# Kernel tuning notes

Hardware: AMD Instinct MI355X
Metric: run time of the kernel (lower is better)

The kernel has to match this reference:

```python
import jax, jax.numpy as jnp
import numpy as np

B, T, E = 2, 4096, 1024
N_HEAD, DIM_HEAD = 16, 64
BUCKET_SIZE, N_HASHES = 64, 4
N_LOCAL = 4
DIM_FF = 4096
TOKEN_SELF_VAL = -5e4
LN_EPS = 1e-5


def _mask_val(dtype):
    return -jnp.finfo(dtype).max


def layer_norm(x, g, b):
    mu = x.mean(-1, keepdims=True)
    var = ((x - mu) ** 2).mean(-1, keepdims=True)
    return (x - mu) / jnp.sqrt(var + LN_EPS) * g + b


def lsh_attend(qk, v, rotations):
    # qk, v: (bh, t, d). Faithful port of reformer_pytorch LSHAttention
    # (causal, attend_across_buckets=True, allow_duplicate_attention=True).
    bh, t, d = qk.shape
    nb = t // BUCKET_SIZE  # n_buckets
    # --- hash vectors ---
    rotated = jnp.einsum('btf,fhi->bhti', qk, rotations)  # (bh,H,t,nb//2)
    rotated = jnp.concatenate([rotated, -rotated], axis=-1)
    buckets = jnp.argmax(rotated, axis=-1)  # (bh,H,t)
    offsets = (jnp.arange(N_HASHES) * nb).reshape(1, -1, 1)
    buckets = (buckets + offsets).reshape(bh, -1)  # (bh, H*t)
    # --- sort by (bucket, time) ---
    ticker = jnp.arange(N_HASHES * t)
    buckets_and_t = t * buckets + (ticker[None, :] % t)
    sticker = jnp.argsort(buckets_and_t, axis=-1)  # (bh, H*t)
    undo = jnp.argsort(sticker, axis=-1)
    st = sticker % t
    sqk = jnp.take_along_axis(qk, st[:, :, None], axis=1)
    sv = jnp.take_along_axis(v, st[:, :, None], axis=1)
    chunks = N_HASHES * nb
    bq_t = st.reshape(bh, chunks, BUCKET_SIZE)
    bqk = sqk.reshape(bh, chunks, BUCKET_SIZE, d)
    bv = sv.reshape(bh, chunks, BUCKET_SIZE, d)
    bq = bqk
    bk = bqk / jnp.linalg.norm(bqk, axis=-1, keepdims=True)  # normalize keys

    def look_one_back(x):
        extra = jnp.concatenate([x[:, -1:], x[:, :-1]], axis=1)
        return jnp.concatenate([x, extra], axis=2)

    bk = look_one_back(bk)
    bv = look_one_back(bv)
    bkv_t = look_one_back(bq_t)
    dots = jnp.einsum('bcie,bcje->bcij', bq, bk) * (d ** -0.5)
    mval = _mask_val(dots.dtype)
    dots = jnp.where(bq_t[:, :, :, None] < bkv_t[:, :, None, :], mval, dots)  # causal
    dots = jnp.where(bq_t[:, :, :, None] == bkv_t[:, :, None, :], TOKEN_SELF_VAL, dots)
    lse = jax.scipy.special.logsumexp(dots, axis=-1, keepdims=True)
    p = jnp.exp(dots - lse)
    bo = jnp.einsum('bcij,bcje->bcie', p, bv)
    so = bo.reshape(bh, -1, d)
    slog = lse.reshape(bh, -1)
    o = jnp.take_along_axis(so, undo[:, :, None], axis=1)
    logits = jnp.take_along_axis(slog, undo, axis=1)
    o = o.reshape(bh, N_HASHES, t, d)
    logits = logits.reshape(bh, N_HASHES, t, 1)
    probs = jnp.exp(logits - jax.scipy.special.logsumexp(logits, axis=1, keepdims=True))
    return jnp.sum(o * probs, axis=1)  # (bh, t, d)


def local_attend(q, k, v):
    # local-attention with shared_qk=True, causal, window=2*bucket_size,
    # look_backward=1, look_forward=0.
    b, t, e = q.shape
    w = 2 * BUCKET_SIZE
    nw = t // w
    k = k / jnp.linalg.norm(k, axis=-1, keepdims=True)
    b_t = jnp.arange(t).reshape(1, nw, w)
    bq = q.reshape(b, nw, w, e)
    bk = k.reshape(b, nw, w, e)
    bv = v.reshape(b, nw, w, e)

    def look_around(x, pad_value):
        pads = [(0, 0), (1, 0)] + [(0, 0)] * (x.ndim - 2)
        padded = jnp.pad(x, pads, constant_values=pad_value)
        return jnp.concatenate([padded[:, :-1], padded[:, 1:]], axis=2)  # [prev, cur]

    bk = look_around(bk, 0.0)
    bv = look_around(bv, 0.0)
    bq_k = look_around(b_t, -1)
    dots = jnp.einsum('bwie,bwje->bwij', bq, bk) * (e ** -0.5)
    mval = _mask_val(dots.dtype)
    dots = jnp.where(b_t[:, :, :, None] == bq_k[:, :, None, :], TOKEN_SELF_VAL, dots)
    dots = jnp.where(b_t[:, :, :, None] < bq_k[:, :, None, :], mval, dots)
    dots = jnp.where((bq_k == -1)[:, :, None, :], mval, dots)
    attn = jax.nn.softmax(dots, axis=-1)
    out = jnp.einsum('bwij,bwje->bwie', attn, bv)
    return out.reshape(b, t, e)


def _block(x, w_qk, w_v, w_out, b_out, w_ff1, b_ff1, w_ff2, b_ff2,
           ln1_g, ln1_b, ln2_g, ln2_b, rotations):
    b, t, e = x.shape
    qk = x @ w_qk.T
    v = x @ w_v.T
    # split heads: (b,t,e) -> (b,h,t,dh)
    qk = qk.reshape(b, t, N_HEAD, DIM_HEAD).transpose(0, 2, 1, 3)
    v = v.reshape(b, t, N_HEAD, DIM_HEAD).transpose(0, 2, 1, 3)
    lsh_h = N_HEAD - N_LOCAL
    lqk = qk[:, :N_LOCAL].reshape(b * N_LOCAL, t, DIM_HEAD)
    lv = v[:, :N_LOCAL].reshape(b * N_LOCAL, t, DIM_HEAD)
    qk_l = qk[:, N_LOCAL:].reshape(b * lsh_h, t, DIM_HEAD)
    v_l = v[:, N_LOCAL:].reshape(b * lsh_h, t, DIM_HEAD)
    out_lsh = lsh_attend(qk_l, v_l, rotations).reshape(b, lsh_h, t, DIM_HEAD)
    out_loc = local_attend(lqk, lqk, lv).reshape(b, N_LOCAL, t, DIM_HEAD)
    out = jnp.concatenate([out_loc, out_lsh], axis=1)  # local heads first
    out = out.transpose(0, 2, 1, 3).reshape(b, t, e)
    sa = out @ w_out.T + b_out
    x = layer_norm(x + sa, ln1_g, ln1_b)
    h = jax.nn.gelu(x @ w_ff1.T + b_ff1, approximate=False)
    ff = h @ w_ff2.T + b_ff2
    return layer_norm(x + ff, ln2_g, ln2_b)


def setup_inputs() -> dict:
    key = jax.random.key(0)
    ks = jax.random.split(key, 8)
    s = 0.02
    return {
        'x': jax.random.normal(ks[0], (B, T, E), jnp.float32),
        'w_qk': s * jax.random.normal(ks[1], (E, E), jnp.float32),
        'w_v': s * jax.random.normal(ks[2], (E, E), jnp.float32),
        'w_out': s * jax.random.normal(ks[3], (E, E), jnp.float32),
        'b_out': jnp.zeros((E,), jnp.float32),
        'w_ff1': s * jax.random.normal(ks[4], (DIM_FF, E), jnp.float32),
        'b_ff1': jnp.zeros((DIM_FF,), jnp.float32),
        'w_ff2': s * jax.random.normal(ks[5], (E, DIM_FF), jnp.float32),
        'b_ff2': jnp.zeros((E,), jnp.float32),
        'ln1_g': jnp.ones((E,), jnp.float32),
        'ln1_b': jnp.zeros((E,), jnp.float32),
        'ln2_g': jnp.ones((E,), jnp.float32),
        'ln2_b': jnp.zeros((E,), jnp.float32),
        'rotations': jax.random.normal(ks[6], (DIM_HEAD, N_HASHES, (T // BUCKET_SIZE) // 2), jnp.float32),
    }


def reference(x, w_qk, w_v, w_out, b_out, w_ff1, b_ff1, w_ff2, b_ff2,
              ln1_g, ln1_b, ln2_g, ln2_b, rotations):
    return _block(x, w_qk, w_v, w_out, b_out, w_ff1, b_ff1, w_ff2, b_ff2,
                  ln1_g, ln1_b, ln2_g, ln2_b, rotations)
```

## Files before the change

kernel.cpp:

```cpp
#include <hip/hip_runtime.h>
#include <math.h>


#define TSEQ 4096
#define EMB  1024
#define HT   16384
#define GAP_EPS 1.2e-5f

__device__ __forceinline__ ushort f2bf_rne(float f) {
  unsigned int u = __float_as_uint(f);
  u += 0x7fffu + ((u >> 16) & 1u);
  return (ushort)(u >> 16);
}
__device__ __forceinline__ float bf2f(ushort h) {
  return __uint_as_float(((unsigned int)h) << 16);
}

typedef __attribute__((ext_vector_type(8))) short bfrag8;
typedef __attribute__((ext_vector_type(4))) float accf4;

__device__ __forceinline__ void glds16(const ushort* g, ushort* l) {
  __builtin_amdgcn_global_load_lds(
      (const __attribute__((address_space(1))) unsigned int*)g,
      (__attribute__((address_space(3))) unsigned int*)l, 16, 0, 0);
}

__global__ __launch_bounds__(256) void split2_kernel(
    const float4* __restrict__ s, ushort4* __restrict__ h,
    ushort4* __restrict__ l, int n4) {
  int i = blockIdx.x * 256 + threadIdx.x;
  int st = gridDim.x * 256;
  for (; i < n4; i += st) {
    float4 v = s[i];
    ushort4 hh, ll;
    hh.x = f2bf_rne(v.x); ll.x = f2bf_rne(v.x - bf2f(hh.x));
    hh.y = f2bf_rne(v.y); ll.y = f2bf_rne(v.y - bf2f(hh.y));
    hh.z = f2bf_rne(v.z); ll.z = f2bf_rne(v.z - bf2f(hh.z));
    hh.w = f2bf_rne(v.w); ll.w = f2bf_rne(v.w - bf2f(hh.w));
    h[i] = hh; l[i] = ll;
  }
}

__global__ __launch_bounds__(256) void split3_kernel(
    const float4* __restrict__ s, ushort4* __restrict__ h,
    ushort4* __restrict__ m, ushort4* __restrict__ l, int n4) {
  int i = blockIdx.x * 256 + threadIdx.x;
  int st = gridDim.x * 256;
  for (; i < n4; i += st) {
    float4 v = s[i];
    ushort4 hh, mm, ll;
    {
      ushort a = f2bf_rne(v.x); float r = v.x - bf2f(a);
      ushort b = f2bf_rne(r);   float r2 = r - bf2f(b);
      hh.x = a; mm.x = b; ll.x = f2bf_rne(r2);
    }
    {
      ushort a = f2bf_rne(v.y); float r = v.y - bf2f(a);
      ushort b = f2bf_rne(r);   float r2 = r - bf2f(b);
      hh.y = a; mm.y = b; ll.y = f2bf_rne(r2);
    }
    {
      ushort a = f2bf_rne(v.z); float r = v.z - bf2f(a);
      ushort b = f2bf_rne(r);   float r2 = r - bf2f(b);
      hh.z = a; mm.z = b; ll.z = f2bf_rne(r2);
    }
    {
      ushort a = f2bf_rne(v.w); float r = v.w - bf2f(a);
      ushort b = f2bf_rne(r);   float r2 = r - bf2f(b);
      hh.w = a; mm.w = b; ll.w = f2bf_rne(r2);
    }
    h[i] = hh; m[i] = mm; l[i] = ll;
  }
}

#define SSTR 136

template<int AT, int BT, int MS, bool BIAS, bool GELU_ACT, bool F32OUT, bool BF16OUT>
__global__ __launch_bounds__(256) void gemm_mfma_bt(
    const ushort* __restrict__ A0, const ushort* __restrict__ A1,
    const ushort* __restrict__ A2,
    const ushort* __restrict__ B0, const ushort* __restrict__ B1,
    const ushort* __restrict__ B2,
    const float* __restrict__ bias, float* __restrict__ C,
    ushort* __restrict__ Cbf,
    int M, int N, int K) {
  constexpr int NMAT = AT + BT;
  constexpr int LDSU0 = NMAT * 4096;
  constexpr int LDSU = (BF16OUT && LDSU0 < 128 * SSTR) ? 128 * SSTR : LDSU0;
  __shared__ ushort smu[LDSU];

  const ushort* As[3] = {A0, A1, A2};
  const ushort* Bs[3] = {B0, B1, B2};

  int tid = threadIdx.x;
  int lane = tid & 63, wave = tid >> 6;

  int bx, by;
  {
    int gx = gridDim.x, gy = gridDim.y;
    int nwg = gx * gy;
    int flat = blockIdx.y * gx + blockIdx.x;
    if ((nwg & 7) == 0 && (gx & 3) == 0 && (gy & 3) == 0) {
      int cpx = nwg >> 3;
      int id = (flat & 7) * cpx + (flat >> 3);
      int sid = id >> 4, within = id & 15;
      int scols = gx >> 2;
      int srow = sid / scols, scol = sid - srow * scols;
      by = srow * 4 + (within >> 2);
      bx = scol * 4 + (within & 3);
    } else {
      bx = blockIdx.x; by = blockIdx.y;
    }
  }
  int m0 = by * 128, n0 = bx * 128;
  int wr = wave >> 1, wc = wave & 1;

  accf4 acc[4][4];
#pragma unroll
  for (int i = 0; i < 4; ++i)
#pragma unroll
    for (int j = 0; j < 4; ++j)
      acc[i][j] = (accf4){0.f, 0.f, 0.f, 0.f};

  int lr = lane & 15, kb = lane >> 4;
  int arow = wr * 64 + lr;
  int brow = wc * 64 + lr;

  int srowL = lane >> 2;
  int scolL = (lane & 3) * 8;

  constexpr int CH = NMAT * 8;
  int nk = K / 32;
  for (int kt = 0; kt < nk; ++kt) {
    int koff = kt * 32;
#pragma unroll
    for (int c = wave; c < CH; c += 4) {
      int mat = c >> 3, sub = c & 7;
      const ushort* src;
      if (mat < AT)
        src = As[mat] + (size_t)(m0 + sub * 16 + srowL) * K + koff + scolL;
      else
        src = Bs[mat - AT] + (size_t)(n0 + sub * 16 + srowL) * K + koff + scolL;
      glds16(src, smu + c * 512);
    }
    __syncthreads();

    bfrag8 af[AT][4], bf[BT][4];
#pragma unroll
    for (int t = 0; t < AT; ++t)
#pragma unroll
      for (int i = 0; i < 4; ++i)
        af[t][i] = *(const bfrag8*)&smu[t * 4096 + (arow + i * 16) * 32 + kb * 8];
#pragma unroll
    for (int t = 0; t < BT; ++t)
#pragma unroll
      for (int i = 0; i < 4; ++i)
        bf[t][i] = *(const bfrag8*)&smu[(AT + t) * 4096 + (brow + i * 16) * 32 + kb * 8];
#pragma unroll
    for (int p = 0; p < AT; ++p)
#pragma unroll
      for (int q = 0; q < BT; ++q) {
        if (p + q <= MS) {
#pragma unroll
          for (int i = 0; i < 4; ++i)
#pragma unroll
            for (int j = 0; j < 4; ++j)
              acc[i][j] = __builtin_amdgcn_mfma_f32_16x16x32_bf16(
                  af[p][i], bf[q][j], acc[i][j], 0, 0, 0);
        }
      }
    __syncthreads();
  }

  int crow = (lane >> 4) * 4;
  int ccol = lane & 15;
  if (!BF16OUT) {
#pragma unroll
    for (int i = 0; i < 4; ++i) {
#pragma unroll
      for (int j = 0; j < 4; ++j) {
#pragma unroll
        for (int r = 0; r < 4; ++r) {
          int m = m0 + wr * 64 + i * 16 + crow + r;
          int n = n0 + wc * 64 + j * 16 + ccol;
          float val = acc[i][j][r];
          if (BIAS) val += bias[n];
          if (GELU_ACT) val = 0.5f * val * (1.f + erff(val * 0.70710678118654752f));
          if (F32OUT) C[(size_t)m * N + n] = val;
        }
      }
    }
  } else {
    ushort* stg = smu;
#pragma unroll
    for (int i = 0; i < 4; ++i) {
#pragma unroll
      for (int j = 0; j < 4; ++j) {
#pragma unroll
        for (int r = 0; r < 4; ++r) {
          int ml = wr * 64 + i * 16 + crow + r;
          int nl = wc * 64 + j * 16 + ccol;
          float val = acc[i][j][r];
          if (BIAS) val += bias[n0 + nl];
          if (GELU_ACT) val = 0.5f * val * (1.f + erff(val * 0.70710678118654752f));
          stg[ml * SSTR + nl] = f2bf_rne(val);
        }
      }
    }
    __syncthreads();
    int rowl = tid >> 1, half = tid & 1;
    const uint4* src = (const uint4*)(stg + rowl * SSTR + half * 64);
    uint4* dst = (uint4*)(Cbf + (size_t)(m0 + rowl) * N + n0 + half * 64);
#pragma unroll
    for (int u = 0; u < 8; ++u) dst[u] = src[u];
  }
}

__global__ __launch_bounds__(256) void hash_kernel(
    const float* __restrict__ qk, const float* __restrict__ rot,
    int* __restrict__ buckets, int* __restrict__ altb,
    float* __restrict__ gapf) {
  int idx = blockIdx.x * 256 + threadIdx.x;
  int t = idx & 4095;
  int bh_h = idx >> 12;
  int h = bh_h & 3;
  int bh = bh_h >> 2;
  int b = bh / 12, hh = bh % 12;
  const float* qrow = qk + ((size_t)(b * TSEQ + t) * EMB + (4 + hh) * 64);
  double q[64]; double qn2 = 0.0;
#pragma unroll
  for (int f = 0; f < 64; ++f) { q[f] = (double)qrow[f]; qn2 += q[f] * q[f]; }
  double r[32];
  for (int i = 0; i < 32; ++i) {
    double acc = 0.0;
#pragma unroll
    for (int f = 0; f < 64; ++f)
      acc = fma(q[f], (double)rot[f * 128 + h * 32 + i], acc);
    r[i] = acc;
  }
  double best1 = -1e300, best2 = -1e300; int j1 = 0, j2 = 0;
  for (int j = 0; j < 64; ++j) {
    double val = (j < 32) ? r[j] : -r[j - 32];
    if (val > best1) { best2 = best1; j2 = j1; best1 = val; j1 = j; }
    else if (val > best2) { best2 = val; j2 = j; }
  }
  buckets[idx] = j1 + h * 64;
  altb[idx]    = j2 + h * 64;
  gapf[idx] = (float)((best1 - best2) / sqrt(qn2 + 1e-300));
}

__global__ __launch_bounds__(256) void mkalt_kernel(
    const int* __restrict__ buckets, const int* __restrict__ altb,
    const float* __restrict__ gapf, int* __restrict__ buckets1) {
  int idx = blockIdx.x * 256 + threadIdx.x;
  buckets1[idx] = (gapf[idx] < GAP_EPS) ? altb[idx] : buckets[idx];
}

__global__ __launch_bounds__(64) void sort_kernel(
    const int* __restrict__ buckets, int* __restrict__ stime,
    int* __restrict__ undo) {
  int bh = blockIdx.x >> 8;
  int bucket = blockIdx.x & 255;
  int h = bucket >> 6;
  int lane = threadIdx.x;
  const int* row = buckets + (size_t)bh * HT;
  int cnt = 0;
  for (int base = 0; base < HT; base += 64)
    cnt += (row[base + lane] < bucket) ? 1 : 0;
#pragma unroll
  for (int off = 1; off < 64; off <<= 1) cnt += __shfl_xor(cnt, off);
  int offset = cnt;
  const int* hrow = row + h * 4096;
  for (int t0 = 0; t0 < 4096; t0 += 64) {
    bool match = (hrow[t0 + lane] == bucket);
    unsigned long long m = __ballot(match);
    int pre = __popcll(m & ((1ull << lane) - 1ull));
    if (match) {
      int pos = offset + pre;
      int time = t0 + lane;
      stime[(size_t)bh * HT + pos] = time;
      undo[(size_t)bh * HT + h * 4096 + time] = pos;
    }
    offset += __popcll(m);
  }
}

#define KSTR  88
#define VSTR 152

__global__ __launch_bounds__(256) void lsh_attend_mfma_kernel(
    const float* __restrict__ qk, const float* __restrict__ v,
    const int* __restrict__ stime, float* __restrict__ so,
    float* __restrict__ slog) {
  __shared__ ushort KS[128 * KSTR];
  __shared__ ushort VT[64 * VSTR];
  __shared__ int tks[128];
  __shared__ float qn[64];
  ushort* PS = KS;

  int bh = blockIdx.x >> 8;
  int c = blockIdx.x & 255;
  int prev = (c + 255) & 255;
  int b = bh / 12, hh = bh % 12;
  int col0 = (4 + hh) * 64;
  int tid = threadIdx.x;
  int lane = tid & 63;
  int wave = tid >> 6;

  if (tid < 128) {
    int src = (tid < 64) ? c : prev;
    tks[tid] = stime[(size_t)bh * HT + src * 64 + (tid & 63)];
  }
  __syncthreads();

  if (tid < 128) {
    int r = tid;
    const float* kr = qk + (size_t)(b * TSEQ + tks[r]) * EMB + col0;
    float row[64]; float ss = 0.f;
#pragma unroll
    for (int f = 0; f < 64; f += 4) {
      float4 t4 = *(const float4*)(kr + f);
      row[f] = t4.x; row[f + 1] = t4.y; row[f + 2] = t4.z; row[f + 3] = t4.w;
      ss += t4.x * t4.x + t4.y * t4.y + t4.z * t4.z + t4.w * t4.w;
    }
    float rn = (ss > 0.f) ? rsqrtf(ss) : 0.f;
    if (r < 64) qn[r] = sqrtf(ss);
#pragma unroll
    for (int f = 0; f < 64; f += 4) {
      ushort4 u;
      u.x = f2bf_rne(row[f] * rn);
      u.y = f2bf_rne(row[f + 1] * rn);
      u.z = f2bf_rne(row[f + 2] * rn);
      u.w = f2bf_rne(row[f + 3] * rn);
      *(ushort4*)&KS[r * KSTR + f] = u;
    }
  } else {
    int kk = tid - 128;
    const float* vr = v + (size_t)(b * TSEQ + tks[kk]) * EMB + col0;
#pragma unroll
    for (int f = 0; f < 64; f += 4) {
      float4 t4 = *(const float4*)(vr + f);
      VT[(f + 0) * VSTR + kk] = f2bf_rne(t4.x);
      VT[(f + 1) * VSTR + kk] = f2bf_rne(t4.y);
      VT[(f + 2) * VSTR + kk] = f2bf_rne(t4.z);
      VT[(f + 3) * VSTR + kk] = f2bf_rne(t4.w);
    }
  }
  __syncthreads();

  int lr = lane & 15, kb = lane >> 4;
  int qrow0 = wave * 16;
  bfrag8 af0 = *(const bfrag8*)&KS[(qrow0 + lr) * KSTR + kb * 8];
  bfrag8 af1 = *(const bfrag8*)&KS[(qrow0 + lr) * KSTR + 32 + kb * 8];
  float d[8][4];
#pragma unroll
  for (int nt = 0; nt < 8; ++nt) {
    bfrag8 b0 = *(const bfrag8*)&KS[(nt * 16 + lr) * KSTR + kb * 8];
    bfrag8 b1 = *(const bfrag8*)&KS[(nt * 16 + lr) * KSTR + 32 + kb * 8];
    accf4 acc = (accf4){0.f, 0.f, 0.f, 0.f};
    acc = __builtin_amdgcn_mfma_f32_16x16x32_bf16(af0, b0, acc, 0, 0, 0);
    acc = __builtin_amdgcn_mfma_f32_16x16x32_bf16(af1, b1, acc, 0, 0, 0);
#pragma unroll
    for (int r = 0; r < 4; ++r) d[nt][r] = acc[r];
  }

  const float mvalf = -3.402823466e38f;
  int crow = kb * 4;
  int tq[4]; float qs[4];
#pragma unroll
  for (int r = 0; r < 4; ++r) {
    tq[r] = tks[qrow0 + crow + r];
    qs[r] = qn[qrow0 + crow + r] * 0.125f;
  }
  float mrow[4] = {mvalf, mvalf, mvalf, mvalf};
#pragma unroll
  for (int nt = 0; nt < 8; ++nt) {
    int tk = tks[nt * 16 + lr];
#pragma unroll
    for (int r = 0; r < 4; ++r) {
      float dv = d[nt][r] * qs[r];
      if (tq[r] < tk) dv = mvalf;
      else if (tq[r] == tk) dv = -5e4f;
      d[nt][r] = dv;
      mrow[r] = fmaxf(mrow[r], dv);
    }
  }
#pragma unroll
  for (int off = 1; off < 16; off <<= 1)
#pragma unroll
    for (int r = 0; r < 4; ++r)
      mrow[r] = fmaxf(mrow[r], __shfl_xor(mrow[r], off));
  float srow[4] = {0.f, 0.f, 0.f, 0.f};
#pragma unroll
  for (int nt = 0; nt < 8; ++nt)
#pragma unroll
    for (int r = 0; r < 4; ++r) {
      float e = expf(d[nt][r] - mrow[r]);
      d[nt][r] = e;
      srow[r] += e;
    }
#pragma unroll
  for (int off = 1; off < 16; off <<= 1)
#pragma unroll
    for (int r = 0; r < 4; ++r)
      srow[r] += __shfl_xor(srow[r], off);
  if (lr == 0) {
#pragma unroll
    for (int r = 0; r < 4; ++r) {
      size_t orow = (size_t)bh * HT + c * 64 + qrow0 + crow + r;
      slog[orow] = mrow[r] + logf(srow[r]);
    }
  }
  float inv[4];
#pragma unroll
  for (int r = 0; r < 4; ++r) inv[r] = 1.f / srow[r];

  __syncthreads();
#pragma unroll
  for (int nt = 0; nt < 8; ++nt)
#pragma unroll
    for (int r = 0; r < 4; ++r)
      PS[(qrow0 + crow + r) * VSTR + nt * 16 + lr] = f2bf_rne(d[nt][r] * inv[r]);
  __syncthreads();

  bfrag8 ap[4];
#pragma unroll
  for (int ks = 0; ks < 4; ++ks)
    ap[ks] = *(const bfrag8*)&PS[(qrow0 + lr) * VSTR + ks * 32 + kb * 8];
#pragma unroll
  for (int nt = 0; nt < 4; ++nt) {
    accf4 acc = (accf4){0.f, 0.f, 0.f, 0.f};
#pragma unroll
    for (int ks = 0; ks < 4; ++ks) {
      bfrag8 bv = *(const bfrag8*)&VT[(nt * 16 + lr) * VSTR + ks * 32 + kb * 8];
      acc = __builtin_amdgcn_mfma_f32_16x16x32_bf16(ap[ks], bv, acc, 0, 0, 0);
    }
#pragma unroll
    for (int r = 0; r < 4; ++r) {
      size_t orow = (size_t)bh * HT + c * 64 + qrow0 + crow + r;
      so[orow * 64 + nt * 16 + lr] = acc[r];
    }
  }
}

__global__ __launch_bounds__(256) void lsh_combine_kernel(
    const float* __restrict__ so, const float* __restrict__ slog,
    const int* __restrict__ undo, float* __restrict__ attn,
    float wnew, float wold) {
  int idx = blockIdx.x * 4 + (threadIdx.x >> 6);
  int lane = threadIdx.x & 63;
  int bh = idx >> 12;
  int t = idx & 4095;
  int b = bh / 12, hh = bh % 12;
  float l[4]; int pos[4];
#pragma unroll
  for (int h = 0; h < 4; ++h) {
    pos[h] = undo[(size_t)bh * HT + h * 4096 + t];
    l[h] = slog[(size_t)bh * HT + pos[h]];
  }
  float m = fmaxf(fmaxf(l[0], l[1]), fmaxf(l[2], l[3]));
  float w[4], s = 0.f;
#pragma unroll
  for (int h = 0; h < 4; ++h) { w[h] = expf(l[h] - m); s += w[h]; }
  float inv = 1.f / s;
  float o = 0.f;
#pragma unroll
  for (int h = 0; h < 4; ++h)
    o += w[h] * inv * so[((size_t)bh * HT + pos[h]) * 64 + lane];
  size_t oi = (size_t)(b * TSEQ + t) * EMB + (4 + hh) * 64 + lane;
  attn[oi] = wold * attn[oi] + wnew * o;
}

#define LKSTR  72
#define LVSTR 264
#define LPSTR 264

__global__ __launch_bounds__(512) void local_attend_mfma_kernel(
    const float* __restrict__ qk, const float* __restrict__ v,
    float* __restrict__ attn) {
  __shared__ ushort KS[256 * LKSTR];
  __shared__ ushort VT[64 * LVSTR];
  __shared__ ushort PS[128 * LPSTR];
  __shared__ float qn[128];
  int row = blockIdx.x >> 5;
  int win = blockIdx.x & 31;
  int b = row >> 2, hl = row & 3;
  int col0 = hl * 64;
  int tid = threadIdx.x;
  int lane = tid & 63, wave = tid >> 6;

  if (tid < 256) {
    int r = tid;
    int t = (r < 128) ? ((win > 0) ? (win - 1) * 128 + r : -1)
                      : (win * 128 + (r - 128));
    if (t >= 0) {
      const float* kr = qk + (size_t)(b * TSEQ + t) * EMB + col0;
      float rowv[64]; float ss = 0.f;
#pragma unroll
      for (int f = 0; f < 64; f += 4) {
        float4 t4 = *(const float4*)(kr + f);
        rowv[f] = t4.x; rowv[f + 1] = t4.y; rowv[f + 2] = t4.z; rowv[f + 3] = t4.w;
        ss += t4.x * t4.x + t4.y * t4.y + t4.z * t4.z + t4.w * t4.w;
      }
      float rn = (ss > 0.f) ? rsqrtf(ss) : 0.f;
      if (r >= 128) qn[r - 128] = sqrtf(ss);
#pragma unroll
      for (int f = 0; f < 64; f += 4) {
        ushort4 u;
        u.x = f2bf_rne(rowv[f] * rn);
        u.y = f2bf_rne(rowv[f + 1] * rn);
        u.z = f2bf_rne(rowv[f + 2] * rn);
        u.w = f2bf_rne(rowv[f + 3] * rn);
        *(ushort4*)&KS[r * LKSTR + f] = u;
      }
    } else {
      ushort4 z = {0, 0, 0, 0};
#pragma unroll
      for (int f = 0; f < 64; f += 4)
        *(ushort4*)&KS[r * LKSTR + f] = z;
    }
  } else {
    int kk = tid - 256;
    int t = (kk < 128) ? ((win > 0) ? (win - 1) * 128 + kk : -1)
                       : (win * 128 + (kk - 128));
    if (t >= 0) {
      const float* vr = v + (size_t)(b * TSEQ + t) * EMB + col0;
#pragma unroll
      for (int f = 0; f < 64; f += 4) {
        float4 t4 = *(const float4*)(vr + f);
        VT[(f + 0) * LVSTR + kk] = f2bf_rne(t4.x);
        VT[(f + 1) * LVSTR + kk] = f2bf_rne(t4.y);
        VT[(f + 2) * LVSTR + kk] = f2bf_rne(t4.z);
        VT[(f + 3) * LVSTR + kk] = f2bf_rne(t4.w);
      }
    } else {
#pragma unroll
      for (int f = 0; f < 64; ++f) VT[f * LVSTR + kk] = 0;
    }
  }
  __syncthreads();

  int lr = lane & 15, kb = lane >> 4;
  int q0 = wave * 16;
  bfrag8 af0 = *(const bfrag8*)&KS[(128 + q0 + lr) * LKSTR + kb * 8];
  bfrag8 af1 = *(const bfrag8*)&KS[(128 + q0 + lr) * LKSTR + 32 + kb * 8];
  float d[16][4];
#pragma unroll
  for (int nt = 0; nt < 16; ++nt) {
    bfrag8 b0 = *(const bfrag8*)&KS[(nt * 16 + lr) * LKSTR + kb * 8];
    bfrag8 b1 = *(const bfrag8*)&KS[(nt * 16 + lr) * LKSTR + 32 + kb * 8];
    accf4 acc = (accf4){0.f, 0.f, 0.f, 0.f};
    acc = __builtin_amdgcn_mfma_f32_16x16x32_bf16(af0, b0, acc, 0, 0, 0);
    acc = __builtin_amdgcn_mfma_f32_16x16x32_bf16(af1, b1, acc, 0, 0, 0);
#pragma unroll
    for (int r = 0; r < 4; ++r) d[nt][r] = acc[r];
  }

  const float mvalf = -3.402823466e38f;
  int crow = kb * 4;
  int tq[4]; float qs[4];
#pragma unroll
  for (int r = 0; r < 4; ++r) {
    int qi = q0 + crow + r;
    tq[r] = win * 128 + qi;
    qs[r] = qn[qi] * 0.125f;
  }
  float mrow[4] = {mvalf, mvalf, mvalf, mvalf};
#pragma unroll
  for (int nt = 0; nt < 16; ++nt) {
    int slot = nt * 16 + lr;
    int tk = (slot < 128) ? ((win > 0) ? (win - 1) * 128 + slot : -1)
                          : (win * 128 + (slot - 128));
#pragma unroll
    for (int r = 0; r < 4; ++r) {
      float dv = d[nt][r] * qs[r];
      if (tk < 0) dv = mvalf;
      else if (tq[r] == tk) dv = -5e4f;
      else if (tq[r] < tk) dv = mvalf;
      d[nt][r] = dv;
      mrow[r] = fmaxf(mrow[r], dv);
    }
  }
#pragma unroll
  for (int off = 1; off < 16; off <<= 1)
#pragma unroll
    for (int r = 0; r < 4; ++r)
      mrow[r] = fmaxf(mrow[r], __shfl_xor(mrow[r], off));
  float srow[4] = {0.f, 0.f, 0.f, 0.f};
#pragma unroll
  for (int nt = 0; nt < 16; ++nt)
#pragma unroll
    for (int r = 0; r < 4; ++r) {
      float e = expf(d[nt][r] - mrow[r]);
      d[nt][r] = e;
      srow[r] += e;
    }
#pragma unroll
  for (int off = 1; off < 16; off <<= 1)
#pragma unroll
    for (int r = 0; r < 4; ++r)
      srow[r] += __shfl_xor(srow[r], off);
  float inv[4];
#pragma unroll
  for (int r = 0; r < 4; ++r) inv[r] = 1.f / srow[r];

#pragma unroll
  for (int nt = 0; nt < 16; ++nt)
#pragma unroll
    for (int r = 0; r < 4; ++r)
      PS[(q0 + crow + r) * LPSTR + nt * 16 + lr] = f2bf_rne(d[nt][r] * inv[r]);
  __syncthreads();

  bfrag8 ap[8];
#pragma unroll
  for (int ks = 0; ks < 8; ++ks)
    ap[ks] = *(const bfrag8*)&PS[(q0 + lr) * LPSTR + ks * 32 + kb * 8];
#pragma unroll
  for (int nt = 0; nt < 4; ++nt) {
    accf4 acc = (accf4){0.f, 0.f, 0.f, 0.f};
#pragma unroll
    for (int ks = 0; ks < 8; ++ks) {
      bfrag8 bv = *(const bfrag8*)&VT[(nt * 16 + lr) * LVSTR + ks * 32 + kb * 8];
      acc = __builtin_amdgcn_mfma_f32_16x16x32_bf16(ap[ks], bv, acc, 0, 0, 0);
    }
#pragma unroll
    for (int r = 0; r < 4; ++r) {
      int tqw = win * 128 + q0 + crow + r;
      attn[(size_t)(b * TSEQ + tqw) * EMB + col0 + nt * 16 + lr] = acc[r];
    }
  }
}

template<bool SPLIT>
__global__ __launch_bounds__(256) void add_ln_kernel(
    const float* __restrict__ a, const float* __restrict__ bsrc,
    const float* __restrict__ g, const float* __restrict__ beta,
    float* __restrict__ out, ushort* __restrict__ ohi,
    ushort* __restrict__ olo) {
  int row = blockIdx.x;
  int tid = threadIdx.x, lane = tid & 63, wave = tid >> 6;
  const float* pa = a + (size_t)row * EMB;
  const float* pb = bsrc + (size_t)row * EMB;
  float xv[4]; float s = 0.f;
#pragma unroll
  for (int u = 0; u < 4; ++u) { int c = tid + u * 256; xv[u] = pa[c] + pb[c]; s += xv[u]; }
#pragma unroll
  for (int off = 1; off < 64; off <<= 1) s += __shfl_xor(s, off);
  __shared__ float red[4];
  __shared__ float red2[4];
  if (lane == 0) red[wave] = s;
  __syncthreads();
  float mu = (red[0] + red[1] + red[2] + red[3]) * (1.f / 1024.f);
  float vs = 0.f;
#pragma unroll
  for (int u = 0; u < 4; ++u) { float dd = xv[u] - mu; vs += dd * dd; }
#pragma unroll
  for (int off = 1; off < 64; off <<= 1) vs += __shfl_xor(vs, off);
  if (lane == 0) red2[wave] = vs;
  __syncthreads();
  float var = (red2[0] + red2[1] + red2[2] + red2[3]) * (1.f / 1024.f);
  float rstd = rsqrtf(var + 1e-5f);
#pragma unroll
  for (int u = 0; u < 4; ++u) {
    int c = tid + u * 256;
    float val = (xv[u] - mu) * rstd * g[c] + beta[c];
    size_t off = (size_t)row * EMB + c;
    out[off] = val;
    if (SPLIT) {
      ushort hh = f2bf_rne(val);
      ohi[off] = hh;
      olo[off] = f2bf_rne(val - bf2f(hh));
    }
  }
}

extern "C" void kernel_launch(void* const* d_in, const int* in_sizes, int n_in,
                              void* d_out, int out_size, void* d_ws, size_t ws_size,
                              hipStream_t stream) {
  (void)in_sizes; (void)n_in; (void)out_size; (void)ws_size;
  const float* x     = (const float*)d_in[0];
  const float* w_qk  = (const float*)d_in[1];
  const float* w_v   = (const float*)d_in[2];
  const float* w_out = (const float*)d_in[3];
  const float* b_out = (const float*)d_in[4];
  const float* w_ff1 = (const float*)d_in[5];
  const float* b_ff1 = (const float*)d_in[6];
  const float* w_ff2 = (const float*)d_in[7];
  const float* b_ff2 = (const float*)d_in[8];
  const float* ln1_g = (const float*)d_in[9];
  const float* ln1_b = (const float*)d_in[10];
  const float* ln2_g = (const float*)d_in[11];
  const float* ln2_b = (const float*)d_in[12];
  const float* rot   = (const float*)d_in[13];
  float* out = (float*)d_out;

  float* ws = (float*)d_ws;
  const size_t SZ = (size_t)8192 * 1024;
  float* qk   = ws;
  float* v    = ws + SZ;
  float* attn = ws + 2 * SZ;
  float* big  = ws + 3 * SZ;
  float* so   = big;
  float* slog = big + (size_t)24 * HT * 64;
  int*   buckets  = (int*)(slog + (size_t)24 * HT);
  int*   stimep   = buckets + (size_t)24 * HT;
  int*   undop    = stimep + (size_t)24 * HT;
  int*   altb     = undop + (size_t)24 * HT;
  float* gapf     = (float*)(altb + (size_t)24 * HT);
  int*   buckets1 = (int*)(gapf + (size_t)24 * HT);
  float* sa  = qk;
  float* x1  = v;
  float* ffo = attn;

  const size_t M4 = 4194304;
  ushort* xs_h  = (ushort*)big;
  ushort* xs_m  = (ushort*)(big + M4);
  ushort* xs_l  = (ushort*)(big + 2 * M4);
  ushort* wqk_h = (ushort*)(big + 3 * M4);
  ushort* wqk_m = (ushort*)(big + 3 * M4 + 524288);
  ushort* wqk_l = (ushort*)(big + 3 * M4 + 2 * 524288);
  ushort* wv_h  = (ushort*)(big + 3 * M4 + 3 * 524288);
  ushort* wv_l  = (ushort*)(big + 3 * M4 + 4 * 524288);
  ushort* attn_h = (ushort*)big;
  ushort* attn_l = (ushort*)(big + M4);
  ushort* wout_h = (ushort*)v;
  ushort* wout_l = (ushort*)(v + 524288);
  ushort* x1_h  = (ushort*)attn;
  ushort* x1_l  = (ushort*)(attn + M4);
  ushort* wff1_h = (ushort*)qk;
  ushort* wff1_l = (ushort*)(qk + 2097152);
  ushort* wff2_h = (ushort*)(qk + 2 * 2097152);
  ushort* wff2_l = (ushort*)(qk + 3 * 2097152);
  ushort* ffh_h = (ushort*)big;

  dim3 blk256(256), blk64(64), blk512(512);
  dim3 g1024(8, 64), g4096(32, 64);

  split3_kernel<<<2048, blk256, 0, stream>>>((const float4*)x, (ushort4*)xs_h,
      (ushort4*)xs_m, (ushort4*)xs_l, 2097152);
  split3_kernel<<<1024, blk256, 0, stream>>>((const float4*)w_qk, (ushort4*)wqk_h,
      (ushort4*)wqk_m, (ushort4*)wqk_l, 262144);
  split2_kernel<<<1024, blk256, 0, stream>>>((const float4*)w_v, (ushort4*)wv_h,
      (ushort4*)wv_l, 262144);
  gemm_mfma_bt<3, 3, 2, false, false, true, false><<<g1024, blk256, 0, stream>>>(
      xs_h, xs_m, xs_l, wqk_h, wqk_m, wqk_l, nullptr, qk, nullptr,
      8192, 1024, 1024);
  gemm_mfma_bt<2, 2, 1, false, false, true, false><<<g1024, blk256, 0, stream>>>(
      xs_h, xs_m, nullptr, wv_h, wv_l, nullptr, nullptr, v, nullptr,
      8192, 1024, 1024);
  hash_kernel<<<1536, blk256, 0, stream>>>(qk, rot, buckets, altb, gapf);
  mkalt_kernel<<<1536, blk256, 0, stream>>>(buckets, altb, gapf, buckets1);

  sort_kernel<<<6144, blk64, 0, stream>>>(buckets, stimep, undop);
  lsh_attend_mfma_kernel<<<6144, blk256, 0, stream>>>(qk, v, stimep, so, slog);
  lsh_combine_kernel<<<24576, blk256, 0, stream>>>(so, slog, undop, attn, 1.0f, 0.0f);
  sort_kernel<<<6144, blk64, 0, stream>>>(buckets1, stimep, undop);
  lsh_attend_mfma_kernel<<<6144, blk256, 0, stream>>>(qk, v, stimep, so, slog);
  lsh_combine_kernel<<<24576, blk256, 0, stream>>>(so, slog, undop, attn, 0.5f, 0.5f);

  local_attend_mfma_kernel<<<256, blk512, 0, stream>>>(qk, v, attn);

  split2_kernel<<<2048, blk256, 0, stream>>>((const float4*)attn, (ushort4*)attn_h,
      (ushort4*)attn_l, 2097152);
  split2_kernel<<<1024, blk256, 0, stream>>>((const float4*)w_out, (ushort4*)wout_h,
      (ushort4*)wout_l, 262144);
  gemm_mfma_bt<2, 2, 1, true, false, true, false><<<g1024, blk256, 0, stream>>>(
      attn_h, attn_l, nullptr, wout_h, wout_l, nullptr, b_out, sa, nullptr,
      8192, 1024, 1024);
  add_ln_kernel<true><<<8192, blk256, 0, stream>>>(x, sa, ln1_g, ln1_b, x1, x1_h, x1_l);
  split2_kernel<<<2048, blk256, 0, stream>>>((const float4*)w_ff1, (ushort4*)wff1_h,
      (ushort4*)wff1_l, 1048576);
  split2_kernel<<<2048, blk256, 0, stream>>>((const float4*)w_ff2, (ushort4*)wff2_h,
      (ushort4*)wff2_l, 1048576);
  gemm_mfma_bt<2, 2, 1, true, true, false, true><<<g4096, blk256, 0, stream>>>(
      x1_h, x1_l, nullptr, wff1_h, wff1_l, nullptr, b_ff1, nullptr, ffh_h,
      8192, 4096, 1024);
  gemm_mfma_bt<1, 2, 1, true, false, true, false><<<g1024, blk256, 0, stream>>>(
      ffh_h, nullptr, nullptr, wff2_h, wff2_l, nullptr, b_ff2, ffo, nullptr,
      8192, 1024, 4096);
  add_ln_kernel<false><<<8192, blk256, 0, stream>>>(x1, ffo, ln2_g, ln2_b, out,
      nullptr, nullptr);
}
```

Measured before the change: 1.176 ms.

## Emit bf16 qk/v from projections and cut split-precision terms in GEMMs

The QK projection now writes both fp32 and a bf16 copy, and the V projection writes only bf16 with fewer split terms. The LSH and local attention kernels read these bf16 operands directly instead of fp32, which halves their gather traffic and drops the per-element conversions. The output projection and FF1 GEMMs lose one split-precision term (the low part of W_out and of x1), and add_ln no longer writes the low bf16 half. The LSH attention grid is also swizzled so that consecutive blocks spread across heads. The cost is lower precision in several places, which risks failing the accuracy tolerance.

```diff
diff --git a/kernel.cpp b/kernel.cpp
--- a/kernel.cpp
+++ b/kernel.cpp
@@ -203,6 +203,7 @@
           float val = acc[i][j][r];
           if (BIAS) val += bias[n0 + nl];
           if (GELU_ACT) val = 0.5f * val * (1.f + erff(val * 0.70710678118654752f));
+          if (F32OUT) C[(size_t)(m0 + ml) * N + n0 + nl] = val;
           stg[ml * SSTR + nl] = f2bf_rne(val);
         }
       }
@@ -289,7 +290,7 @@
 #define VSTR 152
 
 __global__ __launch_bounds__(256) void lsh_attend_mfma_kernel(
-    const float* __restrict__ qk, const float* __restrict__ v,
+    const ushort* __restrict__ qkb, const ushort* __restrict__ vb,
     const int* __restrict__ stime, float* __restrict__ so,
     float* __restrict__ slog) {
   __shared__ ushort KS[128 * KSTR];
@@ -298,8 +299,9 @@
   __shared__ float qn[64];
   ushort* PS = KS;
 
-  int bh = blockIdx.x >> 8;
-  int c = blockIdx.x & 255;
+  int sw = (blockIdx.x & 7) * 768 + (blockIdx.x >> 3);
+  int bh = sw >> 8;
+  int c = sw & 255;
   int prev = (c + 255) & 255;
   int b = bh / 12, hh = bh % 12;
   int col0 = (4 + hh) * 64;
@@ -315,13 +317,16 @@
 
   if (tid < 128) {
     int r = tid;
-    const float* kr = qk + (size_t)(b * TSEQ + tks[r]) * EMB + col0;
+    const ushort* kr = qkb + (size_t)(b * TSEQ + tks[r]) * EMB + col0;
     float row[64]; float ss = 0.f;
 #pragma unroll
-    for (int f = 0; f < 64; f += 4) {
-      float4 t4 = *(const float4*)(kr + f);
-      row[f] = t4.x; row[f + 1] = t4.y; row[f + 2] = t4.z; row[f + 3] = t4.w;
-      ss += t4.x * t4.x + t4.y * t4.y + t4.z * t4.z + t4.w * t4.w;
+    for (int f = 0; f < 64; f += 8) {
+      uint4 u4 = *(const uint4*)(kr + f);
+      const ushort* us = (const ushort*)&u4;
+#pragma unroll
+      for (int q = 0; q < 8; ++q) {
+        float x = bf2f(us[q]); row[f + q] = x; ss += x * x;
+      }
     }
     float rn = (ss > 0.f) ? rsqrtf(ss) : 0.f;
     if (r < 64) qn[r] = sqrtf(ss);
@@ -336,14 +341,14 @@
     }
   } else {
     int kk = tid - 128;
-    const float* vr = v + (size_t)(b * TSEQ + tks[kk]) * EMB + col0;
-#pragma unroll
-    for (int f = 0; f < 64; f += 4) {
-      float4 t4 = *(const float4*)(vr + f);
-      VT[(f + 0) * VSTR + kk] = f2bf_rne(t4.x);
-      VT[(f + 1) * VSTR + kk] = f2bf_rne(t4.y);
-      VT[(f + 2) * VSTR + kk] = f2bf_rne(t4.z);
-      VT[(f + 3) * VSTR + kk] = f2bf_rne(t4.w);
+    const ushort* vr = vb + (size_t)(b * TSEQ + tks[kk]) * EMB + col0;
+#pragma unroll
+    for (int f = 0; f < 64; f += 8) {
+      uint4 u4 = *(const uint4*)(vr + f);
+      const ushort* us = (const ushort*)&u4;
+#pragma unroll
+      for (int q = 0; q < 8; ++q)
+        VT[(f + q) * VSTR + kk] = us[q];
     }
   }
   __syncthreads();
@@ -476,7 +481,7 @@
 #define LPSTR 264
 
 __global__ __launch_bounds__(512) void local_attend_mfma_kernel(
-    const float* __restrict__ qk, const float* __restrict__ v,
+    const ushort* __restrict__ qkb, const ushort* __restrict__ vb,
     float* __restrict__ attn) {
   __shared__ ushort KS[256 * LKSTR];
   __shared__ ushort VT[64 * LVSTR];
@@ -494,13 +499,16 @@
     int t = (r < 128) ? ((win > 0) ? (win - 1) * 128 + r : -1)
                       : (win * 128 + (r - 128));
     if (t >= 0) {
-      const float* kr = qk + (size_t)(b * TSEQ + t) * EMB + col0;
+      const ushort* kr = qkb + (size_t)(b * TSEQ + t) * EMB + col0;
       float rowv[64]; float ss = 0.f;
 #pragma unroll
-      for (int f = 0; f < 64; f += 4) {
-        float4 t4 = *(const float4*)(kr + f);
-        rowv[f] = t4.x; rowv[f + 1] = t4.y; rowv[f + 2] = t4.z; rowv[f + 3] = t4.w;
-        ss += t4.x * t4.x + t4.y * t4.y + t4.z * t4.z + t4.w * t4.w;
+      for (int f = 0; f < 64; f += 8) {
+        uint4 u4 = *(const uint4*)(kr + f);
+        const ushort* us = (const ushort*)&u4;
+#pragma unroll
+        for (int q = 0; q < 8; ++q) {
+          float x = bf2f(us[q]); rowv[f + q] = x; ss += x * x;
+        }
       }
       float rn = (ss > 0.f) ? rsqrtf(ss) : 0.f;
       if (r >= 128) qn[r - 128] = sqrtf(ss);
@@ -524,14 +532,14 @@
     int t = (kk < 128) ? ((win > 0) ? (win - 1) * 128 + kk : -1)
                        : (win * 128 + (kk - 128));
     if (t >= 0) {
-      const float* vr = v + (size_t)(b * TSEQ + t) * EMB + col0;
-#pragma unroll
-      for (int f = 0; f < 64; f += 4) {
-        float4 t4 = *(const float4*)(vr + f);
-        VT[(f + 0) * LVSTR + kk] = f2bf_rne(t4.x);
-        VT[(f + 1) * LVSTR + kk] = f2bf_rne(t4.y);
-        VT[(f + 2) * LVSTR + kk] = f2bf_rne(t4.z);
-        VT[(f + 3) * LVSTR + kk] = f2bf_rne(t4.w);
+      const ushort* vr = vb + (size_t)(b * TSEQ + t) * EMB + col0;
+#pragma unroll
+      for (int f = 0; f < 64; f += 8) {
+        uint4 u4 = *(const uint4*)(vr + f);
+        const ushort* us = (const ushort*)&u4;
+#pragma unroll
+        for (int q = 0; q < 8; ++q)
+          VT[(f + q) * LVSTR + kk] = us[q];
       }
     } else {
 #pragma unroll
@@ -635,8 +643,7 @@
 __global__ __launch_bounds__(256) void add_ln_kernel(
     const float* __restrict__ a, const float* __restrict__ bsrc,
     const float* __restrict__ g, const float* __restrict__ beta,
-    float* __restrict__ out, ushort* __restrict__ ohi,
-    ushort* __restrict__ olo) {
+    float* __restrict__ out, ushort* __restrict__ ohi) {
   int row = blockIdx.x;
   int tid = threadIdx.x, lane = tid & 63, wave = tid >> 6;
   const float* pa = a + (size_t)row * EMB;
@@ -666,11 +673,7 @@
     float val = (xv[u] - mu) * rstd * g[c] + beta[c];
     size_t off = (size_t)row * EMB + c;
     out[off] = val;
-    if (SPLIT) {
-      ushort hh = f2bf_rne(val);
-      ohi[off] = hh;
-      olo[off] = f2bf_rne(val - bf2f(hh));
-    }
+    if (SPLIT) ohi[off] = f2bf_rne(val);
   }
 }
 
@@ -713,6 +716,8 @@
   float* ffo = attn;
 
   const size_t M4 = 4194304;
+  ushort* v_bf  = (ushort*)v;
+  ushort* qk_bf = (ushort*)(v + M4);
   ushort* xs_h  = (ushort*)big;
   ushort* xs_m  = (ushort*)(big + M4);
   ushort* xs_l  = (ushort*)(big + 2 * M4);
@@ -726,7 +731,6 @@
   ushort* wout_h = (ushort*)v;
   ushort* wout_l = (ushort*)(v + 524288);
   ushort* x1_h  = (ushort*)attn;
-  ushort* x1_l  = (ushort*)(attn + M4);
   ushort* wff1_h = (ushort*)qk;
   ushort* wff1_l = (ushort*)(qk + 2097152);
   ushort* wff2_h = (ushort*)(qk + 2 * 2097152);
@@ -742,42 +746,42 @@
       (ushort4*)wqk_m, (ushort4*)wqk_l, 262144);
   split2_kernel<<<1024, blk256, 0, stream>>>((const float4*)w_v, (ushort4*)wv_h,
       (ushort4*)wv_l, 262144);
-  gemm_mfma_bt<3, 3, 2, false, false, true, false><<<g1024, blk256, 0, stream>>>(
-      xs_h, xs_m, xs_l, wqk_h, wqk_m, wqk_l, nullptr, qk, nullptr,
+  gemm_mfma_bt<3, 3, 2, false, false, true, true><<<g1024, blk256, 0, stream>>>(
+      xs_h, xs_m, xs_l, wqk_h, wqk_m, wqk_l, nullptr, qk, qk_bf,
       8192, 1024, 1024);
-  gemm_mfma_bt<2, 2, 1, false, false, true, false><<<g1024, blk256, 0, stream>>>(
-      xs_h, xs_m, nullptr, wv_h, wv_l, nullptr, nullptr, v, nullptr,
+  gemm_mfma_bt<2, 1, 1, false, false, false, true><<<g1024, blk256, 0, stream>>>(
+      xs_h, xs_m, nullptr, wv_h, nullptr, nullptr, nullptr, nullptr, v_bf,
       8192, 1024, 1024);
   hash_kernel<<<1536, blk256, 0, stream>>>(qk, rot, buckets, altb, gapf);
   mkalt_kernel<<<1536, blk256, 0, stream>>>(buckets, altb, gapf, buckets1);
 
   sort_kernel<<<6144, blk64, 0, stream>>>(buckets, stimep, undop);
-  lsh_attend_mfma_kernel<<<6144, blk256, 0, stream>>>(qk, v, stimep, so, slog);
+  lsh_attend_mfma_kernel<<<6144, blk256, 0, stream>>>(qk_bf, v_bf, stimep, so, slog);
   lsh_combine_kernel<<<24576, blk256, 0, stream>>>(so, slog, undop, attn, 1.0f, 0.0f);
   sort_kernel<<<6144, blk64, 0, stream>>>(buckets1, stimep, undop);
-  lsh_attend_mfma_kernel<<<6144, blk256, 0, stream>>>(qk, v, stimep, so, slog);
+  lsh_attend_mfma_kernel<<<6144, blk256, 0, stream>>>(qk_bf, v_bf, stimep, so, slog);
   lsh_combine_kernel<<<24576, blk256, 0, stream>>>(so, slog, undop, attn, 0.5f, 0.5f);
 
-  local_attend_mfma_kernel<<<256, blk512, 0, stream>>>(qk, v, attn);
+  local_attend_mfma_kernel<<<256, blk512, 0, stream>>>(qk_bf, v_bf, attn);
 
   split2_kernel<<<2048, blk256, 0, stream>>>((const float4*)attn, (ushort4*)attn_h,
       (ushort4*)attn_l, 2097152);
   split2_kernel<<<1024, blk256, 0, stream>>>((const float4*)w_out, (ushort4*)wout_h,
       (ushort4*)wout_l, 262144);
-  gemm_mfma_bt<2, 2, 1, true, false, true, false><<<g1024, blk256, 0, stream>>>(
-      attn_h, attn_l, nullptr, wout_h, wout_l, nullptr, b_out, sa, nullptr,
+  gemm_mfma_bt<2, 1, 1, true, false, true, false><<<g1024, blk256, 0, stream>>>(
+      attn_h, attn_l, nullptr, wout_h, nullptr, nullptr, b_out, sa, nullptr,
       8192, 1024, 1024);
-  add_ln_kernel<true><<<8192, blk256, 0, stream>>>(x, sa, ln1_g, ln1_b, x1, x1_h, x1_l);
+  add_ln_kernel<true><<<8192, blk256, 0, stream>>>(x, sa, ln1_g, ln1_b, x1, x1_h);
   split2_kernel<<<2048, blk256, 0, stream>>>((const float4*)w_ff1, (ushort4*)wff1_h,
       (ushort4*)wff1_l, 1048576);
   split2_kernel<<<2048, blk256, 0, stream>>>((const float4*)w_ff2, (ushort4*)wff2_h,
       (ushort4*)wff2_l, 1048576);
-  gemm_mfma_bt<2, 2, 1, true, true, false, true><<<g4096, blk256, 0, stream>>>(
-      x1_h, x1_l, nullptr, wff1_h, wff1_l, nullptr, b_ff1, nullptr, ffh_h,
+  gemm_mfma_bt<1, 2, 1, true, true, false, true><<<g4096, blk256, 0, stream>>>(
+      x1_h, nullptr, nullptr, wff1_h, wff1_l, nullptr, b_ff1, nullptr, ffh_h,
       8192, 4096, 1024);
   gemm_mfma_bt<1, 2, 1, true, false, true, false><<<g1024, blk256, 0, stream>>>(
       ffh_h, nullptr, nullptr, wff2_h, wff2_l, nullptr, b_ff2, ffo, nullptr,
       8192, 1024, 4096);
   add_ln_kernel<false><<<8192, blk256, 0, stream>>>(x1, ffo, ln2_g, ln2_b, out,
-      nullptr, nullptr);
-}
+      nullptr);
+}
```

New measurement: 1.125 ms. -4.4%, faster.
